# Performance work log

Hardware: AMD Instinct MI355X
Metric: run time of the kernel (lower is better)

## Reference

```python
import jax, jax.numpy as jnp
import numpy as np

B, T, D = 16, 2048, 1024

def setup_inputs() -> dict:
    key = jax.random.key(0)
    k1, k2, k3 = jax.random.split(key, 3)
    input = jax.random.normal(k1, (B, T, D), dtype=jnp.float32)
    lengths = jax.random.randint(k2, (B,), 0, T, dtype=jnp.int64)
    weights = jax.random.normal(k3, (T,), dtype=jnp.float32)
    return {"input": input, "lengths": lengths, "weights": weights}

def reference(input, lengths, weights):
    # softmax over the learned per-position weights: [T]
    scores = jax.nn.softmax(weights)
    # mask[b, t] = 1 if t < lengths[b] else 0 (zero out padded timesteps)
    mask = (jnp.arange(T)[None, :] < lengths[:, None]).astype(input.dtype)  # [B, T]
    # fused masked softmax-weighted sum over time: [B, D]
    coeff = scores[None, :] * mask  # [B, T]
    return jnp.einsum("btd,bt->bd", input, coeff)
```

## Files before the change

### kernel.cpp

```cpp
#include <hip/hip_runtime.h>

#define B 16
#define T 2048
#define D 1024
#define NSLICE 32
#define SLICE (D / NSLICE)

#define FMA4(c, v, a)                    \
    do {                                 \
        (a).x = fmaf((c), (v).x, (a).x); \
        (a).y = fmaf((c), (v).y, (a).y); \
        (a).z = fmaf((c), (v).z, (a).z); \
        (a).w = fmaf((c), (v).w, (a).w); \
    } while (0)

__global__ __launch_bounds__(256, 4) void fused1_kernel(
    const float* __restrict__ input,
    const int* __restrict__ lengths,
    const float* __restrict__ weights,
    float* __restrict__ out) {
    const int b   = blockIdx.x >> 5;
    const int s   = blockIdx.x & 31;
    const int tid = threadIdx.x;
    const int c   = tid & 7;
    const int rp  = tid >> 3;
    const int len = lengths[b];

    const float4* __restrict__ in4 =
        (const float4*)input + (size_t)b * T * (D / 4) + s * (SLICE / 4) + c;

    float4 acc = make_float4(0.f, 0.f, 0.f, 0.f);

    const int nfull = len >> 5;
    const float*  wr = weights + rp;
    const float4* p  = in4 + (size_t)rp * (D / 4);
#pragma unroll 4
    for (int it = 0; it < nfull; ++it) {
        const float  cw = expf(wr[it * 32]);
        const float4 v  = p[(size_t)it * 32 * (D / 4)];
        FMA4(cw, v, acc);
    }
    const int r = nfull * 32 + rp;
    if (r < len) {
        const float  cw = expf(weights[r]);
        const float4 v  = in4[(size_t)r * (D / 4)];
        FMA4(cw, v, acc);
    }

    float lsum = 0.f;
#pragma unroll
    for (int i = 0; i < 8; ++i)
        lsum += expf(weights[tid * 8 + i]);
#pragma unroll
    for (int off = 32; off > 0; off >>= 1)
        lsum += __shfl_xor(lsum, off);
    __shared__ float red[4];
    if ((tid & 63) == 0) red[tid >> 6] = lsum;
    __syncthreads();
    const float inv = 1.f / (red[0] + red[1] + red[2] + red[3]);

    __shared__ float4 lds[32][8];
    lds[rp][c] = acc;
    __syncthreads();
#pragma unroll
    for (int off = 16; off > 0; off >>= 1) {
        if (rp < off) {
            const float4 o = lds[rp + off][c];
            acc.x += o.x; acc.y += o.y; acc.z += o.z; acc.w += o.w;
            lds[rp][c] = acc;
        }
        __syncthreads();
    }

    if (tid < 8) {
        const float4 r4 = make_float4(acc.x * inv, acc.y * inv,
                                      acc.z * inv, acc.w * inv);
        ((float4*)out)[b * (D / 4) + s * (SLICE / 4) + tid] = r4;
    }
}

extern "C" void kernel_launch(void* const* d_in, const int* in_sizes, int n_in,
                              void* d_out, int out_size, void* d_ws, size_t ws_size,
                              hipStream_t stream) {
    const float* input   = (const float*)d_in[0];
    const int*   lengths = (const int*)d_in[1];
    const float* weights = (const float*)d_in[2];
    float* out = (float*)d_out;

    fused1_kernel<<<B * NSLICE, 256, 0, stream>>>(input, lengths, weights, out);
}
```

Baseline: 18.24 us.

## Balance work across blocks by splitting concatenated valid rows with atomic accumulation

Instead of assigning one block per (batch, slice), each block now takes an equal chunk of the concatenated valid time rows across all batches. A block may span batch boundaries and reduces partial sums per batch, accumulating into the output with atomicAdd. The output is zeroed with a memset before launch. The goal is to remove load imbalance from varying lengths, at the cost of an extra memset, atomics, and a per-segment reduction with more syncs.

```diff
diff --git a/kernel.cpp b/kernel.cpp
--- a/kernel.cpp
+++ b/kernel.cpp
@@ -4,6 +4,7 @@
 #define T 2048
 #define D 1024
 #define NSLICE 32
+#define NJ 32
 #define SLICE (D / NSLICE)
 
 #define FMA4(c, v, a)                    \
@@ -14,38 +15,29 @@
         (a).w = fmaf((c), (v).w, (a).w); \
     } while (0)
 
-__global__ __launch_bounds__(256, 4) void fused1_kernel(
+__global__ __launch_bounds__(256, 4) void fused_bal_kernel(
     const float* __restrict__ input,
     const int* __restrict__ lengths,
     const float* __restrict__ weights,
     float* __restrict__ out) {
-    const int b   = blockIdx.x >> 5;
-    const int s   = blockIdx.x & 31;
+    const int s   = blockIdx.x & (NSLICE - 1);
+    const int j   = blockIdx.x >> 5;
     const int tid = threadIdx.x;
     const int c   = tid & 7;
     const int rp  = tid >> 3;
-    const int len = lengths[b];
 
-    const float4* __restrict__ in4 =
-        (const float4*)input + (size_t)b * T * (D / 4) + s * (SLICE / 4) + c;
-
-    float4 acc = make_float4(0.f, 0.f, 0.f, 0.f);
-
-    const int nfull = len >> 5;
-    const float*  wr = weights + rp;
-    const float4* p  = in4 + (size_t)rp * (D / 4);
-#pragma unroll 4
-    for (int it = 0; it < nfull; ++it) {
-        const float  cw = expf(wr[it * 32]);
-        const float4 v  = p[(size_t)it * 32 * (D / 4)];
-        FMA4(cw, v, acc);
+    int st[B], ln[B];
+    int N = 0;
+#pragma unroll
+    for (int i = 0; i < B; ++i) {
+        ln[i] = lengths[i];
+        st[i] = N;
+        N += ln[i];
     }
-    const int r = nfull * 32 + rp;
-    if (r < len) {
-        const float  cw = expf(weights[r]);
-        const float4 v  = in4[(size_t)r * (D / 4)];
-        FMA4(cw, v, acc);
-    }
+    const int W  = (N + NJ - 1) >> 5;
+    const int g0 = j * W;
+    const int g1 = min(g0 + W, N);
+    if (g0 >= g1) return;
 
     float lsum = 0.f;
 #pragma unroll
@@ -60,22 +52,44 @@
     const float inv = 1.f / (red[0] + red[1] + red[2] + red[3]);
 
     __shared__ float4 lds[32][8];
-    lds[rp][c] = acc;
-    __syncthreads();
+
+    int g = g0;
+#pragma unroll 1
+    for (int i = 0; i < B; ++i) {
+        if (g >= g1) break;
+        if (g >= st[i] + ln[i]) continue;
+        const int t0 = g - st[i];
+        const int t1 = min(g1 - st[i], ln[i]);
+
+        const float4* __restrict__ in4 =
+            (const float4*)input + (size_t)i * T * (D / 4) + s * (SLICE / 4) + c;
+
+        float4 acc = make_float4(0.f, 0.f, 0.f, 0.f);
+#pragma unroll 4
+        for (int t = t0 + rp; t < t1; t += 32) {
+            const float  cw = expf(weights[t]);
+            const float4 v  = in4[(size_t)t * (D / 4)];
+            FMA4(cw, v, acc);
+        }
+
+        lds[rp][c] = acc;
+        __syncthreads();
 #pragma unroll
-    for (int off = 16; off > 0; off >>= 1) {
-        if (rp < off) {
-            const float4 o = lds[rp + off][c];
-            acc.x += o.x; acc.y += o.y; acc.z += o.z; acc.w += o.w;
-            lds[rp][c] = acc;
+        for (int off = 16; off > 0; off >>= 1) {
+            if (rp < off) {
+                const float4 o = lds[rp + off][c];
+                acc.x += o.x; acc.y += o.y; acc.z += o.z; acc.w += o.w;
+                lds[rp][c] = acc;
+            }
+            __syncthreads();
+        }
+        if (tid < SLICE) {
+            const float val = ((const float*)&lds[0][0])[tid];
+            atomicAdd(&out[i * D + s * SLICE + tid], val * inv);
         }
         __syncthreads();
-    }
 
-    if (tid < 8) {
-        const float4 r4 = make_float4(acc.x * inv, acc.y * inv,
-                                      acc.z * inv, acc.w * inv);
-        ((float4*)out)[b * (D / 4) + s * (SLICE / 4) + tid] = r4;
+        g = st[i] + t1;
     }
 }
 
@@ -87,5 +101,6 @@
     const float* weights = (const float*)d_in[2];
     float* out = (float*)d_out;
 
-    fused1_kernel<<<B * NSLICE, 256, 0, stream>>>(input, lengths, weights, out);
+    hipMemsetAsync(out, 0, (size_t)out_size * sizeof(float), stream);
+    fused_bal_kernel<<<NSLICE * NJ, 256, 0, stream>>>(input, lengths, weights, out);
 }
```

Result: slower. 27.53 us (+51.0%).

## Sort batches by length for block scheduling and cache exp weights in LDS

Applied to the files above, without the earlier changes.

Each block now sorts all batch lengths with an in-register odd-even sort and maps block indices to batches so that the longest and shortest batches are interleaved, aiming to balance load across CUs. It also precomputes exp(weights) once per block into shared memory and reuses it in the accumulation loop, instead of calling expf per row inside the streaming loop. The cost is a redundant 16-element sort per block and an extra 8KB of LDS per block, which may reduce occupancy.

```diff
diff --git a/kernel.cpp b/kernel.cpp
--- a/kernel.cpp
+++ b/kernel.cpp
@@ -14,17 +14,48 @@
         (a).w = fmaf((c), (v).w, (a).w); \
     } while (0)
 
-__global__ __launch_bounds__(256, 4) void fused1_kernel(
+__global__ __launch_bounds__(256, 4) void fused2_kernel(
     const float* __restrict__ input,
     const int* __restrict__ lengths,
     const float* __restrict__ weights,
     float* __restrict__ out) {
-    const int b   = blockIdx.x >> 5;
+    const int j   = blockIdx.x >> 5;
     const int s   = blockIdx.x & 31;
     const int tid = threadIdx.x;
     const int c   = tid & 7;
     const int rp  = tid >> 3;
-    const int len = lengths[b];
+
+    unsigned key[B];
+#pragma unroll
+    for (int i = 0; i < B; ++i)
+        key[i] = ((unsigned)lengths[i] << 4) | (unsigned)i;
+#pragma unroll
+    for (int pass = 0; pass < B; ++pass) {
+#pragma unroll
+        for (int i = (pass & 1); i + 1 < B; i += 2) {
+            const unsigned a = key[i], b2 = key[i + 1];
+            if (a < b2) { key[i] = b2; key[i + 1] = a; }
+        }
+    }
+    const unsigned k = (j < 8) ? key[j] : key[23 - j];
+    const int b   = (int)(k & 15u);
+    const int len = (int)(k >> 4);
+
+    __shared__ float cf[T];
+    __shared__ float red[4];
+    float lsum = 0.f;
+#pragma unroll
+    for (int i = 0; i < 8; ++i) {
+        const float e = expf(weights[tid * 8 + i]);
+        cf[tid * 8 + i] = e;
+        lsum += e;
+    }
+#pragma unroll
+    for (int off = 32; off > 0; off >>= 1)
+        lsum += __shfl_xor(lsum, off);
+    if ((tid & 63) == 0) red[tid >> 6] = lsum;
+    __syncthreads();
+    const float inv = 1.f / (red[0] + red[1] + red[2] + red[3]);
 
     const float4* __restrict__ in4 =
         (const float4*)input + (size_t)b * T * (D / 4) + s * (SLICE / 4) + c;
@@ -32,32 +63,19 @@
     float4 acc = make_float4(0.f, 0.f, 0.f, 0.f);
 
     const int nfull = len >> 5;
-    const float*  wr = weights + rp;
-    const float4* p  = in4 + (size_t)rp * (D / 4);
+    const float4* p = in4 + (size_t)rp * (D / 4);
 #pragma unroll 4
     for (int it = 0; it < nfull; ++it) {
-        const float  cw = expf(wr[it * 32]);
+        const float  cw = cf[it * 32 + rp];
         const float4 v  = p[(size_t)it * 32 * (D / 4)];
         FMA4(cw, v, acc);
     }
-    const int r = nfull * 32 + rp;
+    const int r = (nfull << 5) + rp;
     if (r < len) {
-        const float  cw = expf(weights[r]);
+        const float  cw = cf[r];
         const float4 v  = in4[(size_t)r * (D / 4)];
         FMA4(cw, v, acc);
     }
-
-    float lsum = 0.f;
-#pragma unroll
-    for (int i = 0; i < 8; ++i)
-        lsum += expf(weights[tid * 8 + i]);
-#pragma unroll
-    for (int off = 32; off > 0; off >>= 1)
-        lsum += __shfl_xor(lsum, off);
-    __shared__ float red[4];
-    if ((tid & 63) == 0) red[tid >> 6] = lsum;
-    __syncthreads();
-    const float inv = 1.f / (red[0] + red[1] + red[2] + red[3]);
 
     __shared__ float4 lds[32][8];
     lds[rp][c] = acc;
@@ -87,5 +105,5 @@
     const float* weights = (const float*)d_in[2];
     float* out = (float*)d_out;
 
-    fused1_kernel<<<B * NSLICE, 256, 0, stream>>>(input, lengths, weights, out);
+    fused2_kernel<<<B * NSLICE, 256, 0, stream>>>(input, lengths, weights, out);
 }
```

Result: no change. 18.23 us (-0.1%).

## Split time dimension across blocks with full-row loads and separate combine kernel

Applied to the files above, without the earlier changes.

Replaces the per-column-slice kernel with a two-pass scheme: the first kernel assigns each block a contiguous chunk of timesteps for one batch and reads full 4 KB rows with each thread owning a float4 column, writing partial sums to workspace. A second kernel sums the 64 partials per output and applies the softmax normalization. This aims to improve memory coalescing and balance work across variable sequence lengths, at the cost of an extra launch and a workspace round trip.

```diff
diff --git a/kernel.cpp b/kernel.cpp
--- a/kernel.cpp
+++ b/kernel.cpp
@@ -3,8 +3,8 @@
 #define B 16
 #define T 2048
 #define D 1024
-#define NSLICE 32
-#define SLICE (D / NSLICE)
+#define Q 64
+#define NP (B * Q)
 
 #define FMA4(c, v, a)                    \
     do {                                 \
@@ -14,38 +14,40 @@
         (a).w = fmaf((c), (v).w, (a).w); \
     } while (0)
 
-__global__ __launch_bounds__(256, 4) void fused1_kernel(
+__global__ __launch_bounds__(256) void stream_kernel(
     const float* __restrict__ input,
     const int* __restrict__ lengths,
     const float* __restrict__ weights,
-    float* __restrict__ out) {
-    const int b   = blockIdx.x >> 5;
-    const int s   = blockIdx.x & 31;
+    float* __restrict__ ws) {
+    const int b   = blockIdx.x & (B - 1);
+    const int q   = blockIdx.x >> 4;
     const int tid = threadIdx.x;
-    const int c   = tid & 7;
-    const int rp  = tid >> 3;
     const int len = lengths[b];
+    const int nq  = (len + Q - 1) >> 6;
+    const int t0  = q * nq;
+    const int t1  = min(t0 + nq, len);
 
     const float4* __restrict__ in4 =
-        (const float4*)input + (size_t)b * T * (D / 4) + s * (SLICE / 4) + c;
+        (const float4*)input + (size_t)b * T * (D / 4) + tid;
 
     float4 acc = make_float4(0.f, 0.f, 0.f, 0.f);
+#pragma unroll 4
+    for (int t = t0; t < t1; ++t) {
+        const float  c = expf(weights[t]);
+        const float4 v = in4[(size_t)t * (D / 4)];
+        FMA4(c, v, acc);
+    }
+    ((float4*)ws)[(size_t)blockIdx.x * (D / 4) + tid] = acc;
+}
 
-    const int nfull = len >> 5;
-    const float*  wr = weights + rp;
-    const float4* p  = in4 + (size_t)rp * (D / 4);
-#pragma unroll 4
-    for (int it = 0; it < nfull; ++it) {
-        const float  cw = expf(wr[it * 32]);
-        const float4 v  = p[(size_t)it * 32 * (D / 4)];
-        FMA4(cw, v, acc);
-    }
-    const int r = nfull * 32 + rp;
-    if (r < len) {
-        const float  cw = expf(weights[r]);
-        const float4 v  = in4[(size_t)r * (D / 4)];
-        FMA4(cw, v, acc);
-    }
+__global__ __launch_bounds__(256) void combine_kernel(
+    const float* __restrict__ weights,
+    const float* __restrict__ ws,
+    float* __restrict__ out) {
+    const int tid = threadIdx.x;
+    const int b   = blockIdx.x >> 2;
+    const int ds  = blockIdx.x & 3;
+    const int d   = ds * 256 + tid;
 
     float lsum = 0.f;
 #pragma unroll
@@ -59,24 +61,13 @@
     __syncthreads();
     const float inv = 1.f / (red[0] + red[1] + red[2] + red[3]);
 
-    __shared__ float4 lds[32][8];
-    lds[rp][c] = acc;
-    __syncthreads();
-#pragma unroll
-    for (int off = 16; off > 0; off >>= 1) {
-        if (rp < off) {
-            const float4 o = lds[rp + off][c];
-            acc.x += o.x; acc.y += o.y; acc.z += o.z; acc.w += o.w;
-            lds[rp][c] = acc;
-        }
-        __syncthreads();
-    }
+    const float* __restrict__ p = ws + (size_t)b * D + d;
+    float s = 0.f;
+#pragma unroll 8
+    for (int q = 0; q < Q; ++q)
+        s += p[(size_t)q * (B * D)];
 
-    if (tid < 8) {
-        const float4 r4 = make_float4(acc.x * inv, acc.y * inv,
-                                      acc.z * inv, acc.w * inv);
-        ((float4*)out)[b * (D / 4) + s * (SLICE / 4) + tid] = r4;
-    }
+    out[b * D + d] = s * inv;
 }
 
 extern "C" void kernel_launch(void* const* d_in, const int* in_sizes, int n_in,
@@ -86,6 +77,8 @@
     const int*   lengths = (const int*)d_in[1];
     const float* weights = (const float*)d_in[2];
     float* out = (float*)d_out;
+    float* ws  = (float*)d_ws;
 
-    fused1_kernel<<<B * NSLICE, 256, 0, stream>>>(input, lengths, weights, out);
+    stream_kernel<<<NP, 256, 0, stream>>>(input, lengths, weights, ws);
+    combine_kernel<<<B * 4, 256, 0, stream>>>(weights, ws, out);
 }
```

Measured after the change: 24.71 us. 35.5% more time.
